# Kernel optimization log

Measured on AMD Instinct MI355X. Metric: run time of the kernel, lower is better.

The kernel has to match this reference:

```python
import jax, jax.numpy as jnp
import numpy as np

N_OBJ = 20000
N_TRI = 100000
D = 512      # input_dim_obj == input_dim_pred == output_dim
H = 512      # hidden_dim


def _kaiming(key, fan_out, fan_in):
    return jax.random.normal(key, (fan_out, fan_in), jnp.float32) * jnp.sqrt(2.0 / fan_in)


def setup_inputs() -> dict:
    key = jax.random.key(0)
    ks = jax.random.split(key, 12)
    obj_vecs = jax.random.normal(ks[0], (N_OBJ, D), jnp.float32)
    pred_vecs = jax.random.normal(ks[1], (N_TRI, D), jnp.float32)
    edges = jax.random.randint(ks[2], (N_TRI, 2), 0, N_OBJ, jnp.int32)
    Din1 = 2 * D + D            # net1 input: 1536
    Dout1 = 2 * H + D           # net1 output: 1536
    return {
        "obj_vecs": obj_vecs,
        "pred_vecs": pred_vecs,
        "edges": edges,
        "W1": _kaiming(ks[3], H, Din1), "b1": jnp.zeros((H,), jnp.float32),
        "W2": _kaiming(ks[4], Dout1, H), "b2": jnp.zeros((Dout1,), jnp.float32),
        "V1": _kaiming(ks[5], H, H), "c1": jnp.zeros((H,), jnp.float32),
        "V2": _kaiming(ks[6], D, H), "c2": jnp.zeros((D,), jnp.float32),
        "P_obj": jax.random.normal(ks[7], (D, D), jnp.float32) * (1.0 / jnp.sqrt(D)),
        "pb_obj": jnp.zeros((D,), jnp.float32),
        "P_pred": jax.random.normal(ks[8], (D, D), jnp.float32) * (1.0 / jnp.sqrt(D)),
        "pb_pred": jnp.zeros((D,), jnp.float32),
    }


def reference(obj_vecs, pred_vecs, edges, W1, b1, W2, b2, V1, c1, V2, c2,
              P_obj, pb_obj, P_pred, pb_pred):
    num_objs = obj_vecs.shape[0]
    s_idx = edges[:, 0]
    o_idx = edges[:, 1]
    # gather + concat: [T, 2*D + D]
    cur_t = jnp.concatenate([obj_vecs[s_idx], pred_vecs, obj_vecs[o_idx]], axis=1)
    # net1: Linear -> ReLU -> Linear -> ReLU (final_nonlinearity=True)
    h = jax.nn.relu(cur_t @ W1.T + b1)
    new_t = jax.nn.relu(h @ W2.T + b2)            # [T, 2H + D]
    new_s = new_t[:, :H]
    new_p = new_t[:, H:H + D]
    new_o = new_t[:, H + D:2 * H + D]
    # scatter_add pooling
    pooled = jax.ops.segment_sum(new_s, s_idx, num_segments=num_objs)
    pooled = pooled + jax.ops.segment_sum(new_o, o_idx, num_segments=num_objs)
    # avg pooling normalization
    ones = jnp.ones((edges.shape[0],), jnp.float32)
    counts = jax.ops.segment_sum(ones, s_idx, num_segments=num_objs)
    counts = counts + jax.ops.segment_sum(ones, o_idx, num_segments=num_objs)
    counts = jnp.maximum(counts, 1.0)
    pooled = pooled / counts[:, None]
    # net2: Linear -> ReLU -> Linear -> ReLU
    g = jax.nn.relu(pooled @ V1.T + c1)
    new_obj = jax.nn.relu(g @ V2.T + c2)
    # residual projections
    new_obj = new_obj + obj_vecs @ P_obj.T + pb_obj
    new_p = new_p + pred_vecs @ P_pred.T + pb_pred
    return new_obj, new_p
```

## Files before the change

### kernel.cpp

```cpp
#include <hip/hip_runtime.h>
#include <stdint.h>

#define NOBJ 20000
#define NTRI 100000

typedef unsigned short ushort_t;
typedef __attribute__((ext_vector_type(8))) short short8;
typedef __attribute__((ext_vector_type(4))) float float4v;

enum { MODE_H = 0, MODE_T = 1, MODE_G = 2, MODE_OBJ = 3, MODE_PRED = 4 };

__device__ __forceinline__ ushort_t f2bf(float f) {
    union { float f; unsigned int i; } x;
    x.f = f;
    unsigned int r = x.i + 0x7fffu + ((x.i >> 16) & 1u);
    return (ushort_t)(r >> 16);
}

__device__ __forceinline__ void gload_lds16(const ushort_t* g, short8* l) {
    __builtin_amdgcn_global_load_lds((const __attribute__((address_space(1))) void*)g,
                                     (__attribute__((address_space(3))) void*)l,
                                     16, 0, 0);
}

__global__ void __launch_bounds__(256) cvt_k(const float* __restrict__ src,
                                             ushort_t* __restrict__ dst, int n4) {
    int i = blockIdx.x * 256 + threadIdx.x;
    if (i >= n4) return;
    const float4* s4 = (const float4*)src;
    float4 v = s4[i];
    ushort_t o[4] = {f2bf(v.x), f2bf(v.y), f2bf(v.z), f2bf(v.w)};
    *(uint64_t*)(dst + 4 * (size_t)i) = *(const uint64_t*)o;
}

template <int MODE>
__global__ void __launch_bounds__(256)
gtc_gemm(const ushort_t* __restrict__ A, const ushort_t* __restrict__ Bw,
         const float* __restrict__ bias,
         const ushort_t* __restrict__ A2, const ushort_t* __restrict__ B2,
         const float* __restrict__ bias2,
         const int* __restrict__ edges,
         const ushort_t* __restrict__ objv, const ushort_t* __restrict__ predv,
         float* __restrict__ pooled,
         const float* __restrict__ addend,
         void* __restrict__ outv,
         int M, int K)
{
    __shared__ short8 sA[1024];
    __shared__ short8 sB[1024];
    __shared__ int sIdx[128];
    __shared__ int oIdx[128];

    const int tid  = threadIdx.x;
    const int lane = tid & 63;
    const int wave = tid >> 6;
    const int wm   = wave & 1;
    const int wn   = wave >> 1;
    const int quad = lane >> 4;
    const int lr   = lane & 15;
    const int m0   = blockIdx.y * 128;
    const int n0   = blockIdx.x * 128;

    if (MODE == MODE_H) {
        if (tid < 128) {
            int t = m0 + tid;
            if (t >= M) t = M - 1;
            sIdx[tid] = edges[2 * t];
            oIdx[tid] = edges[2 * t + 1];
        }
        __syncthreads();
    }

    float4v acc[4][4];
#pragma unroll
    for (int i = 0; i < 4; ++i)
#pragma unroll
        for (int j = 0; j < 4; ++j)
            acc[i][j] = (float4v){0.f, 0.f, 0.f, 0.f};

    const int npass = (MODE == MODE_OBJ) ? 2 : 1;
    for (int pass = 0; pass < npass; ++pass) {
        const ushort_t* Ap = (pass == 0) ? A : A2;
        const ushort_t* Bp = (pass == 0) ? Bw : B2;

        for (int k0 = 0; k0 < K; k0 += 64) {
            __syncthreads();
#pragma unroll
            for (int i = 0; i < 4; ++i) {
                int g  = i * 256 + tid;
                int kg = g >> 7;
                int m  = g & 127;
                int krow = k0 + kg * 8;
                const ushort_t* src;
                if (MODE == MODE_H) {
                    int t = m0 + m;
                    if (t >= M) t = M - 1;
                    if (krow < 512)
                        src = objv + (size_t)sIdx[m] * 512 + krow;
                    else if (krow < 1024)
                        src = predv + (size_t)t * 512 + (krow - 512);
                    else
                        src = objv + (size_t)oIdx[m] * 512 + (krow - 1024);
                } else {
                    int r = m0 + m;
                    if (r >= M) r = M - 1;
                    src = Ap + (size_t)r * K + krow;
                }
                gload_lds16(src, &sA[g]);
            }
#pragma unroll
            for (int i = 0; i < 4; ++i) {
                int g  = i * 256 + tid;
                int kg = g >> 7;
                int n  = g & 127;
                gload_lds16(Bp + (size_t)(n0 + n) * K + k0 + kg * 8, &sB[g]);
            }
            __syncthreads();

#pragma unroll
            for (int kk = 0; kk < 2; ++kk) {
                short8 af[4], bfv[4];
#pragma unroll
                for (int t = 0; t < 4; ++t)
                    af[t] = sA[(kk * 4 + quad) * 128 + wm * 64 + t * 16 + lr];
#pragma unroll
                for (int t = 0; t < 4; ++t)
                    bfv[t] = sB[(kk * 4 + quad) * 128 + wn * 64 + t * 16 + lr];
#pragma unroll
                for (int ti = 0; ti < 4; ++ti)
#pragma unroll
                    for (int tj = 0; tj < 4; ++tj)
                        acc[ti][tj] = __builtin_amdgcn_mfma_f32_16x16x32_bf16(
                            af[ti], bfv[tj], acc[ti][tj], 0, 0, 0);
            }
        }

        if (MODE == MODE_OBJ && pass == 0) {
#pragma unroll
            for (int tj = 0; tj < 4; ++tj) {
                float b = bias[n0 + wn * 64 + tj * 16 + lr];
#pragma unroll
                for (int ti = 0; ti < 4; ++ti)
#pragma unroll
                    for (int r = 0; r < 4; ++r)
                        acc[ti][tj][r] = fmaxf(acc[ti][tj][r] + b, 0.f);
            }
        }
    }

    int region = 0;
    if (MODE == MODE_T) region = (int)(blockIdx.x >> 2);

    float bcol[4];
#pragma unroll
    for (int tj = 0; tj < 4; ++tj) {
        int col = n0 + wn * 64 + tj * 16 + lr;
        const float* bptr = (MODE == MODE_OBJ) ? bias2 : bias;
        bcol[tj] = bptr[col];
    }

#pragma unroll
    for (int ti = 0; ti < 4; ++ti) {
#pragma unroll
        for (int r = 0; r < 4; ++r) {
            int row = m0 + wm * 64 + ti * 16 + quad * 4 + r;
            if (row >= M) continue;
            int eidx = 0;
            if (MODE == MODE_T && region != 1)
                eidx = (region == 0) ? edges[2 * row] : edges[2 * row + 1];
#pragma unroll
            for (int tj = 0; tj < 4; ++tj) {
                int col = n0 + wn * 64 + tj * 16 + lr;
                float v = acc[ti][tj][r];
                if (MODE == MODE_H || MODE == MODE_G || MODE == MODE_T)
                    v = fmaxf(v + bcol[tj], 0.f);
                else
                    v = v + bcol[tj];

                if (MODE == MODE_H || MODE == MODE_G) {
                    ((ushort_t*)outv)[(size_t)row * 512 + col] = f2bf(v);
                } else if (MODE == MODE_T) {
                    int c = col & 511;
                    if (region == 1)
                        ((float*)outv)[(size_t)row * 512 + c] = v;
                    else
                        atomicAdd(&pooled[(size_t)eidx * 512 + c], v);
                } else if (MODE == MODE_OBJ) {
                    ((float*)outv)[(size_t)row * 512 + col] = v;
                } else {
                    v += addend[(size_t)row * 512 + col];
                    ((float*)outv)[(size_t)row * 512 + col] = v;
                }
            }
        }
    }
}

__global__ void counts_k(const int* __restrict__ edges, float* __restrict__ counts, int n2) {
    int i = blockIdx.x * 256 + threadIdx.x;
    if (i < n2) atomicAdd(&counts[edges[i]], 1.0f);
}

__global__ void norm_k(const float* __restrict__ pooled, const float* __restrict__ counts,
                       ushort_t* __restrict__ pooledn) {
    int i = blockIdx.x * 256 + threadIdx.x;
    float c = fmaxf(counts[i >> 9], 1.0f);
    pooledn[i] = f2bf(pooled[i] / c);
}

extern "C" void kernel_launch(void* const* d_in, const int* in_sizes, int n_in,
                              void* d_out, int out_size, void* d_ws, size_t ws_size,
                              hipStream_t stream) {
    const float* obj    = (const float*)d_in[0];
    const float* pred   = (const float*)d_in[1];
    const int*   edges  = (const int*)d_in[2];
    const float* W1     = (const float*)d_in[3];
    const float* b1     = (const float*)d_in[4];
    const float* W2     = (const float*)d_in[5];
    const float* b2     = (const float*)d_in[6];
    const float* V1     = (const float*)d_in[7];
    const float* c1     = (const float*)d_in[8];
    const float* V2     = (const float*)d_in[9];
    const float* c2     = (const float*)d_in[10];
    const float* Pobj   = (const float*)d_in[11];
    const float* pbobj  = (const float*)d_in[12];
    const float* Ppred  = (const float*)d_in[13];
    const float* pbpred = (const float*)d_in[14];

    char* ws = (char*)d_ws;
    ushort_t* h       = (ushort_t*)(ws + 0);
    ushort_t* bfPred  = (ushort_t*)(ws + 102400000);
    ushort_t* bfObj   = (ushort_t*)(ws + 204800000);
    ushort_t* bfW1    = (ushort_t*)(ws + 225280000);
    ushort_t* bfW2    = (ushort_t*)(ws + 226852864);
    ushort_t* bfV1    = (ushort_t*)(ws + 228425728);
    ushort_t* bfV2    = (ushort_t*)(ws + 228950016);
    ushort_t* bfPobj  = (ushort_t*)(ws + 229474304);
    ushort_t* bfPpred = (ushort_t*)(ws + 229998592);
    float*    counts  = (float*)   (ws + 230522880);
    ushort_t* pooledn = (ushort_t*)(ws + 0);
    ushort_t* gbuf    = (ushort_t*)(ws + 20480000);

    float* out_obj = (float*)d_out;
    float* out_p   = out_obj + (size_t)NOBJ * 512;
    float* pooled  = out_obj;

    hipMemsetAsync(pooled, 0, 40960000, stream);
    hipMemsetAsync(counts, 0, 80000, stream);

    cvt_k<<<dim3(10000), dim3(256), 0, stream>>>(obj,   bfObj,   10240000/4);
    cvt_k<<<dim3(50000), dim3(256), 0, stream>>>(pred,  bfPred,  51200000/4);
    cvt_k<<<dim3(768),   dim3(256), 0, stream>>>(W1,    bfW1,    786432/4);
    cvt_k<<<dim3(768),   dim3(256), 0, stream>>>(W2,    bfW2,    786432/4);
    cvt_k<<<dim3(256),   dim3(256), 0, stream>>>(V1,    bfV1,    262144/4);
    cvt_k<<<dim3(256),   dim3(256), 0, stream>>>(V2,    bfV2,    262144/4);
    cvt_k<<<dim3(256),   dim3(256), 0, stream>>>(Pobj,  bfPobj,  262144/4);
    cvt_k<<<dim3(256),   dim3(256), 0, stream>>>(Ppred, bfPpred, 262144/4);

    counts_k<<<dim3(782), dim3(256), 0, stream>>>(edges, counts, 2 * NTRI);

    gtc_gemm<MODE_H><<<dim3(4, 782), dim3(256), 0, stream>>>(
        nullptr, bfW1, b1, nullptr, nullptr, nullptr,
        edges, bfObj, bfPred, nullptr, nullptr, h, NTRI, 1536);

    gtc_gemm<MODE_T><<<dim3(12, 782), dim3(256), 0, stream>>>(
        h, bfW2, b2, nullptr, nullptr, nullptr,
        edges, nullptr, nullptr, pooled, nullptr, out_p, NTRI, 512);

    norm_k<<<dim3(40000), dim3(256), 0, stream>>>(pooled, counts, pooledn);

    gtc_gemm<MODE_G><<<dim3(4, 157), dim3(256), 0, stream>>>(
        pooledn, bfV1, c1, nullptr, nullptr, nullptr,
        nullptr, nullptr, nullptr, nullptr, nullptr, gbuf, NOBJ, 512);

    gtc_gemm<MODE_OBJ><<<dim3(4, 157), dim3(256), 0, stream>>>(
        gbuf, bfV2, c2, bfObj, bfPobj, pbobj,
        nullptr, nullptr, nullptr, nullptr, nullptr, out_obj, NOBJ, 512);

    gtc_gemm<MODE_PRED><<<dim3(4, 782), dim3(256), 0, stream>>>(
        bfPred, bfPpred, pbpred, nullptr, nullptr, nullptr,
        nullptr, nullptr, nullptr, nullptr, out_p, out_p, NTRI, 512);
}
```

Before: 1.743 ms.

## Replace atomic scatter-add pooling with CSR-sorted row gather and segment reduce

Builds CSR offsets and permutations for subject and object indices using a histogram, a scan and a fill pass. The second net1 GEMM is split into three column-slice launches. The subject and object slices read h rows in sorted order and write bf16 outputs. A per-object wave kernel then sums each object's contiguous rows without atomics and folds the average normalisation into the second pass. The predicate slice now adds the residual projection computed earlier in its epilogue. This removes roughly a hundred million float atomics, at the cost of extra small kernels, re-reading h three times, and summing bf16-rounded values instead of fp32.

After: 1.714 ms. Within noise of the previous version (-1.7%).

```diff
diff --git a/kernel.cpp b/kernel.cpp
--- a/kernel.cpp
+++ b/kernel.cpp
@@ -8,7 +8,7 @@
 typedef __attribute__((ext_vector_type(8))) short short8;
 typedef __attribute__((ext_vector_type(4))) float float4v;
 
-enum { MODE_H = 0, MODE_T = 1, MODE_G = 2, MODE_OBJ = 3, MODE_PRED = 4 };
+enum { MODE_H = 0, MODE_G = 2, MODE_OBJ = 3, MODE_PRED = 4, MODE_SO = 5, MODE_P = 6 };
 
 __device__ __forceinline__ ushort_t f2bf(float f) {
     union { float f; unsigned int i; } x;
@@ -33,18 +33,112 @@
     *(uint64_t*)(dst + 4 * (size_t)i) = *(const uint64_t*)o;
 }
 
+__global__ void __launch_bounds__(256) hist_k(const int* __restrict__ edges,
+                                              int* __restrict__ counts_s,
+                                              int* __restrict__ counts_o, int n2) {
+    int i = blockIdx.x * 256 + threadIdx.x;
+    if (i >= n2) return;
+    int obj = edges[i];
+    if (i & 1) atomicAdd(&counts_o[obj], 1);
+    else       atomicAdd(&counts_s[obj], 1);
+}
+
+__global__ void __launch_bounds__(256) scan_k(const int* __restrict__ counts,
+                                              int* __restrict__ offs,
+                                              int* __restrict__ cur, int n) {
+    __shared__ int lds[256];
+    const int CHUNK = 80;
+    int t = threadIdx.x;
+    int base = t * CHUNK;
+    int s = 0;
+    for (int j = 0; j < CHUNK; ++j) {
+        int i = base + j;
+        if (i < n) s += counts[i];
+    }
+    lds[t] = s;
+    __syncthreads();
+    for (int off = 1; off < 256; off <<= 1) {
+        int v = (t >= off) ? lds[t - off] : 0;
+        __syncthreads();
+        lds[t] += v;
+        __syncthreads();
+    }
+    int run = lds[t] - s;
+    for (int j = 0; j < CHUNK; ++j) {
+        int i = base + j;
+        if (i < n) {
+            offs[i] = run;
+            cur[i] = run;
+            run += counts[i];
+        } else if (i == n) {
+            offs[n] = run;
+        }
+    }
+}
+
+__global__ void __launch_bounds__(256) fill_k(const int* __restrict__ edges,
+                                              int* __restrict__ cur_s, int* __restrict__ cur_o,
+                                              int* __restrict__ perm_s, int* __restrict__ perm_o,
+                                              int n) {
+    int t = blockIdx.x * 256 + threadIdx.x;
+    if (t >= n) return;
+    int s = edges[2 * t];
+    int o = edges[2 * t + 1];
+    perm_s[atomicAdd(&cur_s[s], 1)] = t;
+    perm_o[atomicAdd(&cur_o[o], 1)] = t;
+}
+
+template <int PASS>
+__global__ void __launch_bounds__(256)
+pool_k(const ushort_t* __restrict__ nst, const int* __restrict__ offs_s,
+       const int* __restrict__ offs_o, float* __restrict__ pooled) {
+    int wave = threadIdx.x >> 6;
+    int lane = threadIdx.x & 63;
+    int obj = blockIdx.x * 4 + wave;
+    if (obj >= NOBJ) return;
+    const int* offs = (PASS == 0) ? offs_s : offs_o;
+    int s = offs[obj], e = offs[obj + 1];
+    float acc[8];
+#pragma unroll
+    for (int j = 0; j < 8; ++j) acc[j] = 0.f;
+    for (int i = s; i < e; ++i) {
+        uint4 v = *(const uint4*)(nst + (size_t)i * 512 + lane * 8);
+        acc[0] += __uint_as_float(v.x << 16);
+        acc[1] += __uint_as_float(v.x & 0xffff0000u);
+        acc[2] += __uint_as_float(v.y << 16);
+        acc[3] += __uint_as_float(v.y & 0xffff0000u);
+        acc[4] += __uint_as_float(v.z << 16);
+        acc[5] += __uint_as_float(v.z & 0xffff0000u);
+        acc[6] += __uint_as_float(v.w << 16);
+        acc[7] += __uint_as_float(v.w & 0xffff0000u);
+    }
+    float* prow = pooled + (size_t)obj * 512 + lane * 8;
+    if (PASS == 0) {
+        *(float4*)(prow)     = make_float4(acc[0], acc[1], acc[2], acc[3]);
+        *(float4*)(prow + 4) = make_float4(acc[4], acc[5], acc[6], acc[7]);
+    } else {
+        float4 a0 = *(const float4*)(prow);
+        float4 a1 = *(const float4*)(prow + 4);
+        int deg = (offs_s[obj + 1] - offs_s[obj]) + (offs_o[obj + 1] - offs_o[obj]);
+        float inv = 1.f / (float)((deg > 1) ? deg : 1);
+        *(float4*)(prow)     = make_float4((acc[0] + a0.x) * inv, (acc[1] + a0.y) * inv,
+                                           (acc[2] + a0.z) * inv, (acc[3] + a0.w) * inv);
+        *(float4*)(prow + 4) = make_float4((acc[4] + a1.x) * inv, (acc[5] + a1.y) * inv,
+                                           (acc[6] + a1.z) * inv, (acc[7] + a1.w) * inv);
+    }
+}
+
 template <int MODE>
 __global__ void __launch_bounds__(256)
 gtc_gemm(const ushort_t* __restrict__ A, const ushort_t* __restrict__ Bw,
          const float* __restrict__ bias,
          const ushort_t* __restrict__ A2, const ushort_t* __restrict__ B2,
          const float* __restrict__ bias2,
-         const int* __restrict__ edges,
+         const int* __restrict__ idx,
          const ushort_t* __restrict__ objv, const ushort_t* __restrict__ predv,
-         float* __restrict__ pooled,
          const float* __restrict__ addend,
          void* __restrict__ outv,
-         int M, int K)
+         int M, int K, int lda)
 {
     __shared__ short8 sA[1024];
     __shared__ short8 sB[1024];
@@ -65,8 +159,15 @@
         if (tid < 128) {
             int t = m0 + tid;
             if (t >= M) t = M - 1;
-            sIdx[tid] = edges[2 * t];
-            oIdx[tid] = edges[2 * t + 1];
+            sIdx[tid] = idx[2 * t];
+            oIdx[tid] = idx[2 * t + 1];
+        }
+        __syncthreads();
+    } else if (MODE == MODE_SO) {
+        if (tid < 128) {
+            int t = m0 + tid;
+            if (t >= M) t = M - 1;
+            sIdx[tid] = idx[t];
         }
         __syncthreads();
     }
@@ -101,10 +202,12 @@
                         src = predv + (size_t)t * 512 + (krow - 512);
                     else
                         src = objv + (size_t)oIdx[m] * 512 + (krow - 1024);
+                } else if (MODE == MODE_SO) {
+                    src = Ap + (size_t)sIdx[m] * (size_t)K + krow;
                 } else {
                     int r = m0 + m;
                     if (r >= M) r = M - 1;
-                    src = Ap + (size_t)r * K + krow;
+                    src = Ap + (size_t)r * (size_t)lda + krow;
                 }
                 gload_lds16(src, &sA[g]);
             }
@@ -148,9 +251,6 @@
         }
     }
 
-    int region = 0;
-    if (MODE == MODE_T) region = (int)(blockIdx.x >> 2);
-
     float bcol[4];
 #pragma unroll
     for (int tj = 0; tj < 4; ++tj) {
@@ -165,47 +265,26 @@
         for (int r = 0; r < 4; ++r) {
             int row = m0 + wm * 64 + ti * 16 + quad * 4 + r;
             if (row >= M) continue;
-            int eidx = 0;
-            if (MODE == MODE_T && region != 1)
-                eidx = (region == 0) ? edges[2 * row] : edges[2 * row + 1];
 #pragma unroll
             for (int tj = 0; tj < 4; ++tj) {
                 int col = n0 + wn * 64 + tj * 16 + lr;
                 float v = acc[ti][tj][r];
-                if (MODE == MODE_H || MODE == MODE_G || MODE == MODE_T)
+                if (MODE == MODE_H || MODE == MODE_G || MODE == MODE_SO) {
                     v = fmaxf(v + bcol[tj], 0.f);
-                else
+                    ((ushort_t*)outv)[(size_t)row * 512 + col] = f2bf(v);
+                } else if (MODE == MODE_P) {
+                    v = fmaxf(v + bcol[tj], 0.f) + addend[(size_t)row * 512 + col];
+                    ((float*)outv)[(size_t)row * 512 + col] = v;
+                } else if (MODE == MODE_OBJ) {
+                    ((float*)outv)[(size_t)row * 512 + col] = v + bcol[tj];
+                } else {
                     v = v + bcol[tj];
-
-                if (MODE == MODE_H || MODE == MODE_G) {
-                    ((ushort_t*)outv)[(size_t)row * 512 + col] = f2bf(v);
-                } else if (MODE == MODE_T) {
-                    int c = col & 511;
-                    if (region == 1)
-                        ((float*)outv)[(size_t)row * 512 + c] = v;
-                    else
-                        atomicAdd(&pooled[(size_t)eidx * 512 + c], v);
-                } else if (MODE == MODE_OBJ) {
-                    ((float*)outv)[(size_t)row * 512 + col] = v;
-                } else {
-                    v += addend[(size_t)row * 512 + col];
+                    if (addend) v += addend[(size_t)row * 512 + col];
                     ((float*)outv)[(size_t)row * 512 + col] = v;
                 }
             }
         }
     }
-}
-
-__global__ void counts_k(const int* __restrict__ edges, float* __restrict__ counts, int n2) {
-    int i = blockIdx.x * 256 + threadIdx.x;
-    if (i < n2) atomicAdd(&counts[edges[i]], 1.0f);
-}
-
-__global__ void norm_k(const float* __restrict__ pooled, const float* __restrict__ counts,
-                       ushort_t* __restrict__ pooledn) {
-    int i = blockIdx.x * 256 + threadIdx.x;
-    float c = fmaxf(counts[i >> 9], 1.0f);
-    pooledn[i] = f2bf(pooled[i] / c);
 }
 
 extern "C" void kernel_launch(void* const* d_in, const int* in_sizes, int n_in,
@@ -230,54 +309,74 @@
     char* ws = (char*)d_ws;
     ushort_t* h       = (ushort_t*)(ws + 0);
     ushort_t* bfPred  = (ushort_t*)(ws + 102400000);
+    ushort_t* nst     = bfPred;
     ushort_t* bfObj   = (ushort_t*)(ws + 204800000);
     ushort_t* bfW1    = (ushort_t*)(ws + 225280000);
+    char* csr = ws + 225280000;
+    int* counts_s = (int*)(csr + 0);
+    int* counts_o = (int*)(csr + 80000);
+    int* offs_s   = (int*)(csr + 160000);
+    int* offs_o   = (int*)(csr + 240064);
+    int* cur_s    = (int*)(csr + 320128);
+    int* cur_o    = (int*)(csr + 400128);
+    int* perm_s   = (int*)(csr + 480128);
+    int* perm_o   = (int*)(csr + 880128);
     ushort_t* bfW2    = (ushort_t*)(ws + 226852864);
     ushort_t* bfV1    = (ushort_t*)(ws + 228425728);
     ushort_t* bfV2    = (ushort_t*)(ws + 228950016);
     ushort_t* bfPobj  = (ushort_t*)(ws + 229474304);
     ushort_t* bfPpred = (ushort_t*)(ws + 229998592);
-    float*    counts  = (float*)   (ws + 230522880);
     ushort_t* pooledn = (ushort_t*)(ws + 0);
     ushort_t* gbuf    = (ushort_t*)(ws + 20480000);
 
     float* out_obj = (float*)d_out;
     float* out_p   = out_obj + (size_t)NOBJ * 512;
-    float* pooled  = out_obj;
-
-    hipMemsetAsync(pooled, 0, 40960000, stream);
-    hipMemsetAsync(counts, 0, 80000, stream);
-
-    cvt_k<<<dim3(10000), dim3(256), 0, stream>>>(obj,   bfObj,   10240000/4);
-    cvt_k<<<dim3(50000), dim3(256), 0, stream>>>(pred,  bfPred,  51200000/4);
-    cvt_k<<<dim3(768),   dim3(256), 0, stream>>>(W1,    bfW1,    786432/4);
-    cvt_k<<<dim3(768),   dim3(256), 0, stream>>>(W2,    bfW2,    786432/4);
-    cvt_k<<<dim3(256),   dim3(256), 0, stream>>>(V1,    bfV1,    262144/4);
-    cvt_k<<<dim3(256),   dim3(256), 0, stream>>>(V2,    bfV2,    262144/4);
-    cvt_k<<<dim3(256),   dim3(256), 0, stream>>>(Pobj,  bfPobj,  262144/4);
-    cvt_k<<<dim3(256),   dim3(256), 0, stream>>>(Ppred, bfPpred, 262144/4);
-
-    counts_k<<<dim3(782), dim3(256), 0, stream>>>(edges, counts, 2 * NTRI);
+    float* pooled = out_obj;
+
+    cvt_k<<<dim3(10000), dim3(256), 0, stream>>>(obj,   bfObj,   10240000 / 4);
+    cvt_k<<<dim3(50000), dim3(256), 0, stream>>>(pred,  bfPred,  51200000 / 4);
+    cvt_k<<<dim3(768),   dim3(256), 0, stream>>>(W1,    bfW1,    786432 / 4);
+    cvt_k<<<dim3(768),   dim3(256), 0, stream>>>(W2,    bfW2,    786432 / 4);
+    cvt_k<<<dim3(256),   dim3(256), 0, stream>>>(V1,    bfV1,    262144 / 4);
+    cvt_k<<<dim3(256),   dim3(256), 0, stream>>>(V2,    bfV2,    262144 / 4);
+    cvt_k<<<dim3(256),   dim3(256), 0, stream>>>(Pobj,  bfPobj,  262144 / 4);
+    cvt_k<<<dim3(256),   dim3(256), 0, stream>>>(Ppred, bfPpred, 262144 / 4);
+
+    gtc_gemm<MODE_PRED><<<dim3(4, 782), dim3(256), 0, stream>>>(
+        bfPred, bfPpred, pbpred, nullptr, nullptr, nullptr,
+        nullptr, nullptr, nullptr, nullptr, out_p, NTRI, 512, 512);
 
     gtc_gemm<MODE_H><<<dim3(4, 782), dim3(256), 0, stream>>>(
         nullptr, bfW1, b1, nullptr, nullptr, nullptr,
-        edges, bfObj, bfPred, nullptr, nullptr, h, NTRI, 1536);
-
-    gtc_gemm<MODE_T><<<dim3(12, 782), dim3(256), 0, stream>>>(
+        edges, bfObj, bfPred, nullptr, h, NTRI, 1536, 1536);
+
+    hipMemsetAsync(counts_s, 0, 160000, stream);
+    hist_k<<<dim3(782), dim3(256), 0, stream>>>(edges, counts_s, counts_o, 2 * NTRI);
+    scan_k<<<dim3(1), dim3(256), 0, stream>>>(counts_s, offs_s, cur_s, NOBJ);
+    scan_k<<<dim3(1), dim3(256), 0, stream>>>(counts_o, offs_o, cur_o, NOBJ);
+    fill_k<<<dim3(391), dim3(256), 0, stream>>>(edges, cur_s, cur_o, perm_s, perm_o, NTRI);
+
+    gtc_gemm<MODE_SO><<<dim3(4, 782), dim3(256), 0, stream>>>(
         h, bfW2, b2, nullptr, nullptr, nullptr,
-        edges, nullptr, nullptr, pooled, nullptr, out_p, NTRI, 512);
-
-    norm_k<<<dim3(40000), dim3(256), 0, stream>>>(pooled, counts, pooledn);
+        perm_s, nullptr, nullptr, nullptr, nst, NTRI, 512, 512);
+    pool_k<0><<<dim3(5000), dim3(256), 0, stream>>>(nst, offs_s, offs_o, pooled);
+
+    gtc_gemm<MODE_SO><<<dim3(4, 782), dim3(256), 0, stream>>>(
+        h, bfW2 + 1024 * 512, b2 + 1024, nullptr, nullptr, nullptr,
+        perm_o, nullptr, nullptr, nullptr, nst, NTRI, 512, 512);
+    pool_k<1><<<dim3(5000), dim3(256), 0, stream>>>(nst, offs_s, offs_o, pooled);
+
+    gtc_gemm<MODE_P><<<dim3(4, 782), dim3(256), 0, stream>>>(
+        h, bfW2 + 512 * 512, b2 + 512, nullptr, nullptr, nullptr,
+        nullptr, nullptr, nullptr, out_p, out_p, NTRI, 512, 512);
+
+    cvt_k<<<dim3(10000), dim3(256), 0, stream>>>(pooled, pooledn, 10240000 / 4);
 
     gtc_gemm<MODE_G><<<dim3(4, 157), dim3(256), 0, stream>>>(
         pooledn, bfV1, c1, nullptr, nullptr, nullptr,
-        nullptr, nullptr, nullptr, nullptr, nullptr, gbuf, NOBJ, 512);
+        nullptr, nullptr, nullptr, nullptr, gbuf, NOBJ, 512, 512);
 
     gtc_gemm<MODE_OBJ><<<dim3(4, 157), dim3(256), 0, stream>>>(
         gbuf, bfV2, c2, bfObj, bfPobj, pbobj,
-        nullptr, nullptr, nullptr, nullptr, nullptr, out_obj, NOBJ, 512);
-
-    gtc_gemm<MODE_PRED><<<dim3(4, 782), dim3(256), 0, stream>>>(
-        bfPred, bfPpred, pbpred, nullptr, nullptr, nullptr,
-        nullptr, nullptr, nullptr, nullptr, out_p, out_p, NTRI, 512);
-}
+        nullptr, nullptr, nullptr, nullptr, out_obj, NOBJ, 512, 512);
+}
```
